# Kernel tuning notes

Measured on AMD Instinct MI355X. Metric: run time of the kernel, lower is better.

Reference implementation:

```python
import jax, jax.numpy as jnp
import numpy as np

N_NODES = 100000
N_EDGES = 1600000
IN_FEATS = 128
OUT_FEATS = 128


def setup_inputs() -> dict:
    key = jax.random.key(0)
    k1, k2, k3, k4, k5 = jax.random.split(key, 5)
    feature = jax.random.normal(k1, (N_NODES, IN_FEATS), dtype=jnp.float32)
    src = jax.random.randint(k2, (N_EDGES,), 0, N_NODES, dtype=jnp.int64)
    dst = jax.random.randint(k3, (N_EDGES,), 0, N_NODES, dtype=jnp.int64)
    # nn.Linear default init: U(-1/sqrt(in), 1/sqrt(in)); randn scaled is fine for a numeric baseline
    bound = 1.0 / np.sqrt(IN_FEATS)
    W = jax.random.uniform(k4, (OUT_FEATS, IN_FEATS), dtype=jnp.float32, minval=-bound, maxval=bound)
    b = jax.random.uniform(k5, (OUT_FEATS,), dtype=jnp.float32, minval=-bound, maxval=bound)
    return {"feature": feature, "src": src, "dst": dst, "W": W, "b": b}


def reference(feature, src, dst, W, b):
    # message passing: copy source feature along each edge, sum into destination node
    agg = jax.ops.segment_sum(feature[src], dst, num_segments=N_NODES)  # [N, in_feats]
    # node apply: ReLU(Linear(h))
    return jax.nn.relu(agg @ W.T + b)  # [N, out_feats]
```

## Files before the change

kernel.cpp:

```cpp
#include <hip/hip_runtime.h>

#define N_NODES 100000
#define N_EDGES 1600000
#define F 128

#define NB    1563
#define NBP2  2048
#define CAP   1280
#define CHUNK 8192

#define BIN_BLOCKS   196
#define HGEMM_BLOCKS 782
#define FRONT_GRID_LIN (BIN_BLOCKS + HGEMM_BLOCKS)

#define LDP  136
#define SMEM_BYTES 77824

typedef __bf16  bf16x8 __attribute__((ext_vector_type(8)));
typedef float   f32x4  __attribute__((ext_vector_type(4)));

__device__ inline unsigned short f32_to_bf16(float f) {
    unsigned u = __builtin_bit_cast(unsigned, f);
    u += 0x7FFFu + ((u >> 16) & 1u);
    return (unsigned short)(u >> 16);
}
__device__ inline unsigned pack_bf16x2(float lo, float hi) {
    return (unsigned)f32_to_bf16(lo) | ((unsigned)f32_to_bf16(hi) << 16);
}
__device__ inline void addrow(float* acc, const uint4 v) {
    acc[0] += __builtin_bit_cast(float, v.x << 16);
    acc[1] += __builtin_bit_cast(float, v.x & 0xFFFF0000u);
    acc[2] += __builtin_bit_cast(float, v.y << 16);
    acc[3] += __builtin_bit_cast(float, v.y & 0xFFFF0000u);
    acc[4] += __builtin_bit_cast(float, v.z << 16);
    acc[5] += __builtin_bit_cast(float, v.z & 0xFFFF0000u);
    acc[6] += __builtin_bit_cast(float, v.w << 16);
    acc[7] += __builtin_bit_cast(float, v.w & 0xFFFF0000u);
}

__global__ __launch_bounds__(1024) void gcn_init(
    const float* __restrict__ W, unsigned short* __restrict__ Wbf,
    int* __restrict__ gcur)
{
    const int i = blockIdx.x * 1024 + threadIdx.x;
    Wbf[i] = f32_to_bf16(W[i]);
    if (i < 1600) gcur[i] = 0;
}

__global__ __launch_bounds__(1024) void gcn_front_lin(
    const float* __restrict__ feat, const unsigned short* __restrict__ Wbf,
    const int* __restrict__ src, const int* __restrict__ dst,
    int* __restrict__ gcur, unsigned* __restrict__ bins,
    unsigned short* __restrict__ H)
{
    __shared__ __align__(16) unsigned char smem[SMEM_BYTES];

    const int tid = threadIdx.x;
    const int bx  = blockIdx.x;

    if (bx >= BIN_BLOCKS) {
        unsigned short* Alds = (unsigned short*)smem;
        unsigned short* Wlds = Alds + 128 * LDP;
        const int row0 = (bx - BIN_BLOCKS) * 128;

        #pragma unroll
        for (int i = 0; i < 2; ++i) {
            const int c = tid + i * 1024;
            const int r = c >> 4, cc = c & 15;
            *(uint4*)&Wlds[r * LDP + cc * 8] = *(const uint4*)&Wbf[c * 8];
        }
        #pragma unroll
        for (int i = 0; i < 4; ++i) {
            const int c = tid + i * 1024;
            const int r = c >> 5, cc = c & 31;
            int gr = row0 + r; if (gr > N_NODES - 1) gr = N_NODES - 1;
            const float4 v = *(const float4*)(feat + (size_t)gr * F + cc * 4);
            uint2 p; p.x = pack_bf16x2(v.x, v.y); p.y = pack_bf16x2(v.z, v.w);
            *(uint2*)&Alds[r * LDP + cc * 4] = p;
        }
        __syncthreads();

        const int lane = tid & 63, wv = tid >> 6;
        const int lr = lane & 15, lq = lane >> 4;
        const int wr = wv & 7;
        const int wc = wv >> 3;

        f32x4 acc[4] = {};
        #pragma unroll
        for (int kk = 0; kk < 4; ++kk) {
            const bf16x8 a = __builtin_bit_cast(bf16x8,
                *(const uint4*)&Alds[(wr * 16 + lr) * LDP + kk * 32 + lq * 8]);
            #pragma unroll
            for (int n2 = 0; n2 < 4; ++n2) {
                const bf16x8 w = __builtin_bit_cast(bf16x8,
                    *(const uint4*)&Wlds[((wc * 4 + n2) * 16 + lr) * LDP + kk * 32 + lq * 8]);
                acc[n2] = __builtin_amdgcn_mfma_f32_16x16x32_bf16(a, w, acc[n2], 0, 0, 0);
            }
        }
        __syncthreads();

        #pragma unroll
        for (int rg = 0; rg < 4; ++rg) {
            const int r = wr * 16 + lq * 4 + rg;
            #pragma unroll
            for (int n2 = 0; n2 < 4; ++n2)
                Alds[r * LDP + (wc * 4 + n2) * 16 + lr] = f32_to_bf16(acc[n2][rg]);
        }
        __syncthreads();

        #pragma unroll
        for (int i = 0; i < 2; ++i) {
            const int c = tid + i * 1024;
            const int r = c >> 4, cc = c & 15;
            const int gr = row0 + r;
            if (gr < N_NODES)
                *(uint4*)(H + (size_t)gr * F + cc * 8) = *(const uint4*)&Alds[r * LDP + cc * 8];
        }
        return;
    }

    unsigned*       cnt    = (unsigned*)smem;
    unsigned*       off    = cnt + NBP2;
    int*            gbase  = (int*)(off + NBP2);
    unsigned*       staged = (unsigned*)(gbase + NBP2);
    unsigned short* sbk    = (unsigned short*)(staged + CHUNK);
    unsigned*       scan   = (unsigned*)(sbk + CHUNK);

    const int e0 = bx * CHUNK;

    #pragma unroll
    for (int i = 0; i < 2; ++i) cnt[tid + i * 1024] = 0;
    __syncthreads();

    int sv[8], dv[8];
    #pragma unroll
    for (int i = 0; i < 8; ++i) {
        const int e = e0 + tid + i * 1024;
        if (e < N_EDGES) {
            sv[i] = src[e];
            dv[i] = dst[e];
            atomicAdd(&cnt[dv[i] >> 6], 1u);
        } else dv[i] = -1;
    }
    __syncthreads();

    const int lane = tid & 63, wid = tid >> 6;
    const unsigned s = cnt[2 * tid] + cnt[2 * tid + 1];
    unsigned v = s;
    #pragma unroll
    for (int o = 1; o < 64; o <<= 1) {
        const unsigned t = __shfl_up(v, o, 64);
        if (lane >= o) v += t;
    }
    if (lane == 63) scan[wid] = v;
    __syncthreads();
    if (tid < 16) {
        const unsigned w = scan[tid];
        unsigned x = w;
        #pragma unroll
        for (int o = 1; o < 16; o <<= 1) {
            const unsigned t = __shfl_up(x, o, 16);
            if (tid >= o) x += t;
        }
        scan[tid] = x - w;
        if (tid == 15) scan[16] = x;
    }
    __syncthreads();
    const unsigned incl = v + scan[wid];
    const unsigned run  = incl - s;
    off[2 * tid]     = run;
    off[2 * tid + 1] = run + cnt[2 * tid];
    __syncthreads();

    #pragma unroll
    for (int i = 0; i < 8; ++i) {
        if (dv[i] >= 0) {
            const int bk = dv[i] >> 6;
            const unsigned w = (unsigned)sv[i] | ((unsigned)(dv[i] & 63) << 17);
            const unsigned p = atomicAdd(&off[bk], 1u);
            staged[p] = w;
            sbk[p] = (unsigned short)bk;
        }
    }
    __syncthreads();

    #pragma unroll
    for (int i = 0; i < 2; ++i) {
        const int bk = 2 * tid + i;
        if (bk < NB && cnt[bk] > 0)
            gbase[bk] = atomicAdd(&gcur[bk], (int)cnt[bk]);
    }
    __syncthreads();

    const int c_tot = (int)scan[16];
    for (int p = tid; p < c_tot; p += 1024) {
        const int bk = sbk[p];
        const int gp = gbase[bk] + (p - (int)(off[bk] - cnt[bk]));
        if (gp < CAP) bins[(size_t)bk * CAP + gp] = staged[p];
    }
}

__global__ __launch_bounds__(512) void gcn_accum_lin(
    const int* __restrict__ gcur,
    const unsigned* __restrict__ bins,
    const unsigned short* __restrict__ H,
    const float* __restrict__ b,
    float* __restrict__ out)
{
    __shared__ unsigned tmp[CAP];
    __shared__ unsigned list[CAP];
    __shared__ int cnt64[64], scn[64], pos64[64], cur64[64];
    __shared__ int nextn;

    const int tid = threadIdx.x;
    const int bkt = blockIdx.x;

    int c = gcur[bkt]; if (c > CAP) c = CAP;
    const unsigned* bb = bins + (size_t)bkt * CAP;

    for (int i = tid; i < c; i += 512) tmp[i] = bb[i];
    if (tid < 64) cnt64[tid] = 0;
    __syncthreads();

    for (int i = tid; i < c; i += 512) atomicAdd(&cnt64[(tmp[i] >> 17) & 63], 1);
    __syncthreads();

    if (tid < 64) scn[tid] = cnt64[tid];
    __syncthreads();
    #pragma unroll
    for (int o = 1; o < 64; o <<= 1) {
        int t = 0;
        if (tid < 64 && tid >= o) t = scn[tid - o];
        __syncthreads();
        if (tid < 64) scn[tid] += t;
        __syncthreads();
    }
    if (tid < 64) {
        const int st = scn[tid] - cnt64[tid];
        pos64[tid] = st;
        cur64[tid] = st;
    }
    if (tid == 0) nextn = 0;
    __syncthreads();

    for (int i = tid; i < c; i += 512) {
        const unsigned w = tmp[i];
        const int p = atomicAdd(&cur64[(w >> 17) & 63], 1);
        list[p] = w;
    }
    __syncthreads();

    const int grp  = tid >> 4;
    const int sl   = tid & 15;
    const int lane = tid & 63;
    const int n0   = bkt * 64;

    for (;;) {
        int myn = 0;
        if (sl == 0) myn = atomicAdd(&nextn, 1);
        myn = __shfl(myn, lane & 48, 64);
        if (myn >= 64) break;

        const int st = pos64[myn];
        const int en = st + cnt64[myn];

        float a0[8] = {0,0,0,0,0,0,0,0};
        float a1[8] = {0,0,0,0,0,0,0,0};
        int k = st;
        for (; k + 7 < en; k += 8) {
            const unsigned w0 = list[k],     w1 = list[k + 1];
            const unsigned w2 = list[k + 2], w3 = list[k + 3];
            const unsigned w4 = list[k + 4], w5 = list[k + 5];
            const unsigned w6 = list[k + 6], w7 = list[k + 7];
            const uint4 v0 = *(const uint4*)(H + (size_t)(w0 & 0x1FFFF) * F + sl * 8);
            const uint4 v1 = *(const uint4*)(H + (size_t)(w1 & 0x1FFFF) * F + sl * 8);
            const uint4 v2 = *(const uint4*)(H + (size_t)(w2 & 0x1FFFF) * F + sl * 8);
            const uint4 v3 = *(const uint4*)(H + (size_t)(w3 & 0x1FFFF) * F + sl * 8);
            const uint4 v4 = *(const uint4*)(H + (size_t)(w4 & 0x1FFFF) * F + sl * 8);
            const uint4 v5 = *(const uint4*)(H + (size_t)(w5 & 0x1FFFF) * F + sl * 8);
            const uint4 v6 = *(const uint4*)(H + (size_t)(w6 & 0x1FFFF) * F + sl * 8);
            const uint4 v7 = *(const uint4*)(H + (size_t)(w7 & 0x1FFFF) * F + sl * 8);
            addrow(a0, v0); addrow(a1, v1); addrow(a0, v2); addrow(a1, v3);
            addrow(a0, v4); addrow(a1, v5); addrow(a0, v6); addrow(a1, v7);
        }
        for (; k + 3 < en; k += 4) {
            const unsigned w0 = list[k],     w1 = list[k + 1];
            const unsigned w2 = list[k + 2], w3 = list[k + 3];
            const uint4 v0 = *(const uint4*)(H + (size_t)(w0 & 0x1FFFF) * F + sl * 8);
            const uint4 v1 = *(const uint4*)(H + (size_t)(w1 & 0x1FFFF) * F + sl * 8);
            const uint4 v2 = *(const uint4*)(H + (size_t)(w2 & 0x1FFFF) * F + sl * 8);
            const uint4 v3 = *(const uint4*)(H + (size_t)(w3 & 0x1FFFF) * F + sl * 8);
            addrow(a0, v0); addrow(a1, v1); addrow(a0, v2); addrow(a1, v3);
        }
        for (; k < en; ++k) {
            const unsigned w0 = list[k];
            const uint4 v0 = *(const uint4*)(H + (size_t)(w0 & 0x1FFFF) * F + sl * 8);
            addrow(a0, v0);
        }
        #pragma unroll
        for (int q = 0; q < 8; ++q) a0[q] += a1[q];

        const int n = n0 + myn;
        if (n < N_NODES) {
            const float4 b0 = *(const float4*)(b + sl * 8);
            const float4 b1 = *(const float4*)(b + sl * 8 + 4);
            float4 o0, o1;
            o0.x = fmaxf(a0[0] + b0.x, 0.0f);
            o0.y = fmaxf(a0[1] + b0.y, 0.0f);
            o0.z = fmaxf(a0[2] + b0.z, 0.0f);
            o0.w = fmaxf(a0[3] + b0.w, 0.0f);
            o1.x = fmaxf(a0[4] + b1.x, 0.0f);
            o1.y = fmaxf(a0[5] + b1.y, 0.0f);
            o1.z = fmaxf(a0[6] + b1.z, 0.0f);
            o1.w = fmaxf(a0[7] + b1.w, 0.0f);
            float* orow = out + (size_t)n * F + sl * 8;
            *(float4*)orow = o0;
            *(float4*)(orow + 4) = o1;
        }
    }
}

#define FEAT_BLOCKS 3125
#define WCONV_BLOCKS 16
#define FRONT_GRID  (BIN_BLOCKS + FEAT_BLOCKS + WCONV_BLOCKS)

__global__ __launch_bounds__(1024) void gcn_front(
    const float* __restrict__ feat, const float* __restrict__ W,
    const int* __restrict__ src, const int* __restrict__ dst,
    int* __restrict__ gcur, unsigned* __restrict__ bins,
    unsigned short* __restrict__ Wbf, float* __restrict__ out)
{
    __shared__ unsigned cnt[NBP2];
    __shared__ unsigned off[NBP2];
    __shared__ int      gbase[NBP2];
    __shared__ unsigned staged[CHUNK];
    __shared__ unsigned short sbk[CHUNK];
    __shared__ unsigned scan[1024];

    const int tid = threadIdx.x;
    const int bx  = blockIdx.x;

    if (bx >= BIN_BLOCKS) {
        const int rb = bx - BIN_BLOCKS;
        if (rb < FEAT_BLOCKS) {
            const int t = rb * 1024 + tid;
            const float4 v = *(const float4*)(feat + (size_t)t * 4);
            uint2 p;
            p.x = pack_bf16x2(v.x, v.y);
            p.y = pack_bf16x2(v.z, v.w);
            const int n = t >> 5, q = t & 31;
            *(uint2*)((char*)out + (size_t)n * 512 + q * 8) = p;
        } else {
            const int i = (rb - FEAT_BLOCKS) * 1024 + tid;
            Wbf[i] = f32_to_bf16(W[i]);
        }
        return;
    }

    const int e0 = bx * CHUNK;

    #pragma unroll
    for (int i = 0; i < 2; ++i) cnt[tid + i * 1024] = 0;
    __syncthreads();

    int sv[8], dv[8];
    #pragma unroll
    for (int i = 0; i < 8; ++i) {
        const int e = e0 + tid + i * 1024;
        if (e < N_EDGES) {
            sv[i] = src[e];
            dv[i] = dst[e];
            atomicAdd(&cnt[dv[i] >> 6], 1u);
        } else dv[i] = -1;
    }
    __syncthreads();

    const unsigned s = cnt[2 * tid] + cnt[2 * tid + 1];
    scan[tid] = s;
    __syncthreads();
    for (int o = 1; o < 1024; o <<= 1) {
        const unsigned t = (tid >= o) ? scan[tid - o] : 0;
        __syncthreads();
        scan[tid] += t;
        __syncthreads();
    }
    const unsigned run = scan[tid] - s;
    off[2 * tid]     = run;
    off[2 * tid + 1] = run + cnt[2 * tid];
    __syncthreads();

    #pragma unroll
    for (int i = 0; i < 8; ++i) {
        if (dv[i] >= 0) {
            const int bk = dv[i] >> 6;
            const unsigned w = (unsigned)sv[i] | ((unsigned)(dv[i] & 63) << 17);
            const unsigned p = atomicAdd(&off[bk], 1u);
            staged[p] = w;
            sbk[p] = (unsigned short)bk;
        }
    }
    __syncthreads();

    #pragma unroll
    for (int i = 0; i < 2; ++i) {
        const int bk = 2 * tid + i;
        if (bk < NB && cnt[bk] > 0)
            gbase[bk] = atomicAdd(&gcur[bk], (int)cnt[bk]);
    }
    __syncthreads();

    const int c_tot = (int)scan[1023];
    for (int p = tid; p < c_tot; p += 1024) {
        const int bk = sbk[p];
        const int gp = gbase[bk] + (p - (int)(off[bk] - cnt[bk]));
        if (gp < CAP) bins[(size_t)bk * CAP + gp] = staged[p];
    }
}

__global__ __launch_bounds__(512) void gcn_accum2(
    const int* __restrict__ gcur,
    const unsigned* __restrict__ bins,
    float* __restrict__ out)
{
    __shared__ unsigned tmp[CAP];
    __shared__ unsigned list[CAP];
    __shared__ int cnt64[64], scn[64], pos64[64], cur64[64];

    const int tid = threadIdx.x;
    const int bkt = blockIdx.x;

    int c = gcur[bkt]; if (c > CAP) c = CAP;
    const unsigned* bb = bins + (size_t)bkt * CAP;

    for (int i = tid; i < c; i += 512) tmp[i] = bb[i];
    if (tid < 64) cnt64[tid] = 0;
    __syncthreads();

    for (int i = tid; i < c; i += 512) atomicAdd(&cnt64[(tmp[i] >> 17) & 63], 1);
    __syncthreads();

    if (tid < 64) scn[tid] = cnt64[tid];
    __syncthreads();
    #pragma unroll
    for (int o = 1; o < 64; o <<= 1) {
        int t = 0;
        if (tid < 64 && tid >= o) t = scn[tid - o];
        __syncthreads();
        if (tid < 64) scn[tid] += t;
        __syncthreads();
    }
    if (tid < 64) {
        const int st = scn[tid] - cnt64[tid];
        pos64[tid] = st;
        cur64[tid] = st;
    }
    __syncthreads();

    for (int i = tid; i < c; i += 512) {
        const unsigned w = tmp[i];
        const int p = atomicAdd(&cur64[(w >> 17) & 63], 1);
        list[p] = w;
    }
    __syncthreads();

    const int grp = tid >> 4;
    const int sl  = tid & 15;
    const int n0  = bkt * 64;

    #pragma unroll
    for (int ni = 0; ni < 2; ++ni) {
        const int l  = grp * 2 + ni;
        const int st = pos64[l];
        const int en = st + cnt64[l];

        float a0[8] = {0,0,0,0,0,0,0,0};
        float a1[8] = {0,0,0,0,0,0,0,0};
        int k = st;
        for (; k + 3 < en; k += 4) {
            const unsigned w0 = list[k],     w1 = list[k + 1];
            const unsigned w2 = list[k + 2], w3 = list[k + 3];
            const uint4 v0 = *(const uint4*)((const char*)out + (size_t)(w0 & 0x1FFFF) * 512 + sl * 16);
            const uint4 v1 = *(const uint4*)((const char*)out + (size_t)(w1 & 0x1FFFF) * 512 + sl * 16);
            const uint4 v2 = *(const uint4*)((const char*)out + (size_t)(w2 & 0x1FFFF) * 512 + sl * 16);
            const uint4 v3 = *(const uint4*)((const char*)out + (size_t)(w3 & 0x1FFFF) * 512 + sl * 16);
            addrow(a0, v0); addrow(a1, v1); addrow(a0, v2); addrow(a1, v3);
        }
        for (; k < en; ++k) {
            const unsigned w0 = list[k];
            const uint4 v0 = *(const uint4*)((const char*)out + (size_t)(w0 & 0x1FFFF) * 512 + sl * 16);
            addrow(a0, v0);
        }
        #pragma unroll
        for (int q = 0; q < 8; ++q) a0[q] += a1[q];

        const int n = n0 + l;
        if (n < N_NODES) {
            uint4 o;
            o.x = pack_bf16x2(a0[0], a0[1]);
            o.y = pack_bf16x2(a0[2], a0[3]);
            o.z = pack_bf16x2(a0[4], a0[5]);
            o.w = pack_bf16x2(a0[6], a0[7]);
            *(uint4*)((char*)out + (size_t)n * 512 + 256 + sl * 16) = o;
        }
    }
}

#define MT   128

__global__ __launch_bounds__(256) void gcn_gemm_mfma(
    float* __restrict__ out,
    const unsigned short* __restrict__ Wbf,
    const float* __restrict__ b)
{
    __shared__ unsigned short Alds[MT * LDP];
    __shared__ unsigned short Wlds[F * LDP];

    const int tid  = threadIdx.x;
    const int row0 = blockIdx.x * MT;

    #pragma unroll
    for (int i = 0; i < 8; ++i) {
        const int c = tid + i * 256;
        const int r = c >> 4, cc = c & 15;
        *(uint4*)&Wlds[r * LDP + cc * 8] = *(const uint4*)&Wbf[c * 8];
    }
    #pragma unroll
    for (int i = 0; i < 8; ++i) {
        const int c = tid + i * 256;
        const int r = c >> 4, cc = c & 15;
        int gr = row0 + r; if (gr > N_NODES - 1) gr = N_NODES - 1;
        const uint4 v = *(const uint4*)((const char*)out + (size_t)gr * 512 + 256 + cc * 16);
        *(uint4*)&Alds[r * LDP + cc * 8] = v;
    }
    __syncthreads();

    const int lane = tid & 63;
    const int wv   = tid >> 6;
    const int lr   = lane & 15;
    const int lq   = lane >> 4;

    f32x4 acc[2][8] = {};
    #pragma unroll
    for (int kk = 0; kk < 4; ++kk) {
        bf16x8 a[2], w[8];
        #pragma unroll
        for (int i = 0; i < 2; ++i)
            a[i] = __builtin_bit_cast(bf16x8,
                *(const uint4*)&Alds[(wv * 32 + i * 16 + lr) * LDP + kk * 32 + lq * 8]);
        #pragma unroll
        for (int n = 0; n < 8; ++n)
            w[n] = __builtin_bit_cast(bf16x8,
                *(const uint4*)&Wlds[(n * 16 + lr) * LDP + kk * 32 + lq * 8]);
        #pragma unroll
        for (int i = 0; i < 2; ++i)
            #pragma unroll
            for (int n = 0; n < 8; ++n)
                acc[i][n] = __builtin_amdgcn_mfma_f32_16x16x32_bf16(a[i], w[n], acc[i][n], 0, 0, 0);
    }

    float bias[8];
    #pragma unroll
    for (int n = 0; n < 8; ++n) bias[n] = b[n * 16 + lr];

    #pragma unroll
    for (int i = 0; i < 2; ++i) {
        const int rbase = wv * 32 + i * 16 + lq * 4;
        #pragma unroll
        for (int rg = 0; rg < 4; ++rg) {
            const int gr = row0 + rbase + rg;
            if (gr < N_NODES) {
                float* orow = out + (size_t)gr * F;
                #pragma unroll
                for (int n = 0; n < 8; ++n) {
                    const float v = acc[i][n][rg] + bias[n];
                    orow[n * 16 + lr] = v > 0.0f ? v : 0.0f;
                }
            }
        }
    }
}

__global__ __launch_bounds__(256) void gcn_scatter(
    const float* __restrict__ feat,
    const int* __restrict__ src, const int* __restrict__ dst,
    float* __restrict__ agg)
{
    const int sub  = threadIdx.x >> 5;
    const int lane = threadIdx.x & 31;
    const long long e = (long long)blockIdx.x * 8 + sub;
    if (e >= N_EDGES) return;
    const int s = src[e], d = dst[e];
    const float4 v = *(const float4*)(feat + (size_t)s * F + lane * 4);
    float* ar = agg + (size_t)d * F + lane * 4;
    unsafeAtomicAdd(ar + 0, v.x);
    unsafeAtomicAdd(ar + 1, v.y);
    unsafeAtomicAdd(ar + 2, v.z);
    unsafeAtomicAdd(ar + 3, v.w);
}

#define GR  64
#define LDW 132
__global__ __launch_bounds__(256) void gcn_gemm_relu(
    float* __restrict__ agg_out,
    const float* __restrict__ W, const float* __restrict__ b)
{
    __shared__ float Wl[F][LDW];
    __shared__ float At[GR][LDW];
    const int tid = threadIdx.x;
    const long long row0 = (long long)blockIdx.x * GR;
    #pragma unroll
    for (int i = 0; i < 64; ++i) {
        const int e = tid + i * 256;
        Wl[e >> 7][e & 127] = W[e];
    }
    #pragma unroll
    for (int i = 0; i < 32; ++i) {
        const int e = tid + i * 256;
        const int r = e >> 7, k2 = e & 127;
        const long long gr = row0 + r;
        At[r][k2] = (gr < N_NODES) ? agg_out[gr * F + k2] : 0.0f;
    }
    __syncthreads();
    const int tx = tid & 15, ty = tid >> 4, r0 = ty * 4;
    float acc[4][8];
    #pragma unroll
    for (int r = 0; r < 4; ++r)
        #pragma unroll
        for (int m = 0; m < 8; ++m) acc[r][m] = 0.0f;
    for (int k0 = 0; k0 < F; k0 += 4) {
        float4 a[4], w[8];
        #pragma unroll
        for (int r = 0; r < 4; ++r) a[r] = *(const float4*)&At[r0 + r][k0];
        #pragma unroll
        for (int m = 0; m < 8; ++m) w[m] = *(const float4*)&Wl[tx + 16 * m][k0];
        #pragma unroll
        for (int r = 0; r < 4; ++r)
            #pragma unroll
            for (int m = 0; m < 8; ++m)
                acc[r][m] += a[r].x * w[m].x + a[r].y * w[m].y
                           + a[r].z * w[m].z + a[r].w * w[m].w;
    }
    float bias[8];
    #pragma unroll
    for (int m = 0; m < 8; ++m) bias[m] = b[tx + 16 * m];
    __syncthreads();
    #pragma unroll
    for (int r = 0; r < 4; ++r) {
        const long long gr = row0 + r0 + r;
        if (gr < N_NODES) {
            float* orow = agg_out + gr * F;
            #pragma unroll
            for (int m = 0; m < 8; ++m) {
                const float v = acc[r][m] + bias[m];
                orow[tx + 16 * m] = v > 0.0f ? v : 0.0f;
            }
        }
    }
}

extern "C" void kernel_launch(void* const* d_in, const int* in_sizes, int n_in,
                              void* d_out, int out_size, void* d_ws, size_t ws_size,
                              hipStream_t stream) {
    const float* feat = (const float*)d_in[0];
    const int*   src  = (const int*)d_in[1];
    const int*   dst  = (const int*)d_in[2];
    const float* W    = (const float*)d_in[3];
    const float* b    = (const float*)d_in[4];
    float* out = (float*)d_out;

    const size_t ws_lin = 1600u * 4 + (size_t)NB * CAP * 4
                        + (size_t)N_NODES * F * 2 + (size_t)F * F * 2;
    const size_t ws_old = 1600u * 4 + (size_t)NB * CAP * 4 + (size_t)F * F * 2;

    if (ws_size >= ws_lin) {
        int* gcur = (int*)d_ws;
        unsigned* bins = (unsigned*)(gcur + 1600);
        unsigned short* H = (unsigned short*)(bins + (size_t)NB * CAP);
        unsigned short* Wbf = H + (size_t)N_NODES * F;

        gcn_init     <<<16, 1024, 0, stream>>>(W, Wbf, gcur);
        gcn_front_lin<<<FRONT_GRID_LIN, 1024, 0, stream>>>(feat, Wbf, src, dst, gcur, bins, H);
        gcn_accum_lin<<<NB, 512, 0, stream>>>(gcur, bins, H, b, out);
    } else if (ws_size >= ws_old) {
        int* gcur = (int*)d_ws;
        unsigned* bins = (unsigned*)(gcur + 1600);
        unsigned short* Wbf = (unsigned short*)(bins + (size_t)NB * CAP);

        hipMemsetAsync(gcur, 0, NB * sizeof(int), stream);
        gcn_front   <<<FRONT_GRID, 1024, 0, stream>>>(feat, W, src, dst, gcur, bins, Wbf, out);
        gcn_accum2  <<<NB, 512, 0, stream>>>(gcur, bins, out);
        gcn_gemm_mfma<<<(N_NODES + MT - 1) / MT, 256, 0, stream>>>(out, Wbf, b);
    } else {
        hipMemsetAsync(out, 0, (size_t)N_NODES * F * sizeof(float), stream);
        gcn_scatter<<<N_EDGES / 8, 256, 0, stream>>>(feat, src, dst, out);
        gcn_gemm_relu<<<(N_NODES + GR - 1) / GR, 256, 0, stream>>>(out, W, b);
    }
}
```

Before: 187.4 us.

## Drop init kernel, convert W in-block, make accum kernel persistent with work stealing

Removes the separate W-to-bf16 init kernel: each H-GEMM block converts W from fp32 itself, and the bucket counters are zeroed with a memset. The accumulate kernel becomes persistent with 1024 blocks that claim buckets through an atomic counter stored in gcur[1599], replacing the shared-memory scan with a wave shuffle scan. Nontemporal loads and stores are added for the streamed data. The intent is to cut launch overhead and tail imbalance, at the cost of redundant W conversion in every GEMM block.

Result: slower. 195.8 us (+4.5%).

```diff
diff --git a/kernel.cpp b/kernel.cpp
--- a/kernel.cpp
+++ b/kernel.cpp
@@ -8,10 +8,12 @@
 #define NBP2  2048
 #define CAP   1280
 #define CHUNK 8192
+#define BCUR  1599
 
 #define BIN_BLOCKS   196
 #define HGEMM_BLOCKS 782
 #define FRONT_GRID_LIN (BIN_BLOCKS + HGEMM_BLOCKS)
+#define ACC_GRID     1024
 
 #define LDP  136
 #define SMEM_BYTES 77824
@@ -38,17 +40,8 @@
     acc[7] += __builtin_bit_cast(float, v.w & 0xFFFF0000u);
 }
 
-__global__ __launch_bounds__(1024) void gcn_init(
-    const float* __restrict__ W, unsigned short* __restrict__ Wbf,
-    int* __restrict__ gcur)
-{
-    const int i = blockIdx.x * 1024 + threadIdx.x;
-    Wbf[i] = f32_to_bf16(W[i]);
-    if (i < 1600) gcur[i] = 0;
-}
-
 __global__ __launch_bounds__(1024) void gcn_front_lin(
-    const float* __restrict__ feat, const unsigned short* __restrict__ Wbf,
+    const float* __restrict__ feat, const float* __restrict__ W,
     const int* __restrict__ src, const int* __restrict__ dst,
     int* __restrict__ gcur, unsigned* __restrict__ bins,
     unsigned short* __restrict__ H)
@@ -64,18 +57,21 @@
         const int row0 = (bx - BIN_BLOCKS) * 128;
 
         #pragma unroll
-        for (int i = 0; i < 2; ++i) {
+        for (int i = 0; i < 4; ++i) {
             const int c = tid + i * 1024;
-            const int r = c >> 4, cc = c & 15;
-            *(uint4*)&Wlds[r * LDP + cc * 8] = *(const uint4*)&Wbf[c * 8];
+            const int r = c >> 5, cc = c & 31;
+            const f32x4 v = *(const f32x4*)(W + (size_t)c * 4);
+            uint2 p; p.x = pack_bf16x2(v[0], v[1]); p.y = pack_bf16x2(v[2], v[3]);
+            *(uint2*)&Wlds[r * LDP + cc * 4] = p;
         }
         #pragma unroll
         for (int i = 0; i < 4; ++i) {
             const int c = tid + i * 1024;
             const int r = c >> 5, cc = c & 31;
             int gr = row0 + r; if (gr > N_NODES - 1) gr = N_NODES - 1;
-            const float4 v = *(const float4*)(feat + (size_t)gr * F + cc * 4);
-            uint2 p; p.x = pack_bf16x2(v.x, v.y); p.y = pack_bf16x2(v.z, v.w);
+            const f32x4 v = __builtin_nontemporal_load(
+                                 (const f32x4*)(feat + (size_t)gr * F + cc * 4));
+            uint2 p; p.x = pack_bf16x2(v[0], v[1]); p.y = pack_bf16x2(v[2], v[3]);
             *(uint2*)&Alds[r * LDP + cc * 4] = p;
         }
         __syncthreads();
@@ -201,7 +197,7 @@
 }
 
 __global__ __launch_bounds__(512) void gcn_accum_lin(
-    const int* __restrict__ gcur,
+    int* __restrict__ gcur,
     const unsigned* __restrict__ bins,
     const unsigned short* __restrict__ H,
     const float* __restrict__ b,
@@ -209,113 +205,120 @@
 {
     __shared__ unsigned tmp[CAP];
     __shared__ unsigned list[CAP];
-    __shared__ int cnt64[64], scn[64], pos64[64], cur64[64];
+    __shared__ int cnt64[64], pos64[64], cur64[64];
+    __shared__ int sbkt;
     __shared__ int nextn;
 
-    const int tid = threadIdx.x;
-    const int bkt = blockIdx.x;
-
-    int c = gcur[bkt]; if (c > CAP) c = CAP;
-    const unsigned* bb = bins + (size_t)bkt * CAP;
-
-    for (int i = tid; i < c; i += 512) tmp[i] = bb[i];
-    if (tid < 64) cnt64[tid] = 0;
-    __syncthreads();
-
-    for (int i = tid; i < c; i += 512) atomicAdd(&cnt64[(tmp[i] >> 17) & 63], 1);
-    __syncthreads();
-
-    if (tid < 64) scn[tid] = cnt64[tid];
-    __syncthreads();
-    #pragma unroll
-    for (int o = 1; o < 64; o <<= 1) {
-        int t = 0;
-        if (tid < 64 && tid >= o) t = scn[tid - o];
-        __syncthreads();
-        if (tid < 64) scn[tid] += t;
-        __syncthreads();
-    }
-    if (tid < 64) {
-        const int st = scn[tid] - cnt64[tid];
-        pos64[tid] = st;
-        cur64[tid] = st;
-    }
-    if (tid == 0) nextn = 0;
-    __syncthreads();
-
-    for (int i = tid; i < c; i += 512) {
-        const unsigned w = tmp[i];
-        const int p = atomicAdd(&cur64[(w >> 17) & 63], 1);
-        list[p] = w;
-    }
-    __syncthreads();
-
-    const int grp  = tid >> 4;
+    const int tid  = threadIdx.x;
+    const int lane = tid & 63;
     const int sl   = tid & 15;
-    const int lane = tid & 63;
-    const int n0   = bkt * 64;
+
+    const f32x4 b0 = *(const f32x4*)(b + sl * 8);
+    const f32x4 b1 = *(const f32x4*)(b + sl * 8 + 4);
 
     for (;;) {
-        int myn = 0;
-        if (sl == 0) myn = atomicAdd(&nextn, 1);
-        myn = __shfl(myn, lane & 48, 64);
-        if (myn >= 64) break;
-
-        const int st = pos64[myn];
-        const int en = st + cnt64[myn];
-
-        float a0[8] = {0,0,0,0,0,0,0,0};
-        float a1[8] = {0,0,0,0,0,0,0,0};
-        int k = st;
-        for (; k + 7 < en; k += 8) {
-            const unsigned w0 = list[k],     w1 = list[k + 1];
-            const unsigned w2 = list[k + 2], w3 = list[k + 3];
-            const unsigned w4 = list[k + 4], w5 = list[k + 5];
-            const unsigned w6 = list[k + 6], w7 = list[k + 7];
-            const uint4 v0 = *(const uint4*)(H + (size_t)(w0 & 0x1FFFF) * F + sl * 8);
-            const uint4 v1 = *(const uint4*)(H + (size_t)(w1 & 0x1FFFF) * F + sl * 8);
-            const uint4 v2 = *(const uint4*)(H + (size_t)(w2 & 0x1FFFF) * F + sl * 8);
-            const uint4 v3 = *(const uint4*)(H + (size_t)(w3 & 0x1FFFF) * F + sl * 8);
-            const uint4 v4 = *(const uint4*)(H + (size_t)(w4 & 0x1FFFF) * F + sl * 8);
-            const uint4 v5 = *(const uint4*)(H + (size_t)(w5 & 0x1FFFF) * F + sl * 8);
-            const uint4 v6 = *(const uint4*)(H + (size_t)(w6 & 0x1FFFF) * F + sl * 8);
-            const uint4 v7 = *(const uint4*)(H + (size_t)(w7 & 0x1FFFF) * F + sl * 8);
-            addrow(a0, v0); addrow(a1, v1); addrow(a0, v2); addrow(a1, v3);
-            addrow(a0, v4); addrow(a1, v5); addrow(a0, v6); addrow(a1, v7);
-        }
-        for (; k + 3 < en; k += 4) {
-            const unsigned w0 = list[k],     w1 = list[k + 1];
-            const unsigned w2 = list[k + 2], w3 = list[k + 3];
-            const uint4 v0 = *(const uint4*)(H + (size_t)(w0 & 0x1FFFF) * F + sl * 8);
-            const uint4 v1 = *(const uint4*)(H + (size_t)(w1 & 0x1FFFF) * F + sl * 8);
-            const uint4 v2 = *(const uint4*)(H + (size_t)(w2 & 0x1FFFF) * F + sl * 8);
-            const uint4 v3 = *(const uint4*)(H + (size_t)(w3 & 0x1FFFF) * F + sl * 8);
-            addrow(a0, v0); addrow(a1, v1); addrow(a0, v2); addrow(a1, v3);
-        }
-        for (; k < en; ++k) {
-            const unsigned w0 = list[k];
-            const uint4 v0 = *(const uint4*)(H + (size_t)(w0 & 0x1FFFF) * F + sl * 8);
-            addrow(a0, v0);
-        }
-        #pragma unroll
-        for (int q = 0; q < 8; ++q) a0[q] += a1[q];
-
-        const int n = n0 + myn;
-        if (n < N_NODES) {
-            const float4 b0 = *(const float4*)(b + sl * 8);
-            const float4 b1 = *(const float4*)(b + sl * 8 + 4);
-            float4 o0, o1;
-            o0.x = fmaxf(a0[0] + b0.x, 0.0f);
-            o0.y = fmaxf(a0[1] + b0.y, 0.0f);
-            o0.z = fmaxf(a0[2] + b0.z, 0.0f);
-            o0.w = fmaxf(a0[3] + b0.w, 0.0f);
-            o1.x = fmaxf(a0[4] + b1.x, 0.0f);
-            o1.y = fmaxf(a0[5] + b1.y, 0.0f);
-            o1.z = fmaxf(a0[6] + b1.z, 0.0f);
-            o1.w = fmaxf(a0[7] + b1.w, 0.0f);
-            float* orow = out + (size_t)n * F + sl * 8;
-            *(float4*)orow = o0;
-            *(float4*)(orow + 4) = o1;
+        __syncthreads();
+        if (tid == 0) {
+            sbkt  = atomicAdd(&gcur[BCUR], 1);
+            nextn = 0;
+        }
+        __syncthreads();
+        const int bkt = sbkt;
+        if (bkt >= NB) return;
+
+        int c = gcur[bkt]; if (c > CAP) c = CAP;
+        const unsigned* bb = bins + (size_t)bkt * CAP;
+
+        for (int i = tid; i < c; i += 512)
+            tmp[i] = __builtin_nontemporal_load(bb + i);
+        if (tid < 64) cnt64[tid] = 0;
+        __syncthreads();
+
+        for (int i = tid; i < c; i += 512) atomicAdd(&cnt64[(tmp[i] >> 17) & 63], 1);
+        __syncthreads();
+
+        if (tid < 64) {
+            const int cv = cnt64[tid];
+            int x = cv;
+            #pragma unroll
+            for (int o = 1; o < 64; o <<= 1) {
+                const int t = __shfl_up(x, o, 64);
+                if (tid >= o) x += t;
+            }
+            pos64[tid] = x - cv;
+            cur64[tid] = x - cv;
+        }
+        __syncthreads();
+
+        for (int i = tid; i < c; i += 512) {
+            const unsigned w = tmp[i];
+            const int p = atomicAdd(&cur64[(w >> 17) & 63], 1);
+            list[p] = w;
+        }
+        __syncthreads();
+
+        const int n0 = bkt * 64;
+
+        for (;;) {
+            int myn = 0;
+            if (sl == 0) myn = atomicAdd(&nextn, 1);
+            myn = __shfl(myn, lane & 48, 64);
+            if (myn >= 64) break;
+
+            const int st = pos64[myn];
+            const int en = st + cnt64[myn];
+
+            float a0[8] = {0,0,0,0,0,0,0,0};
+            float a1[8] = {0,0,0,0,0,0,0,0};
+            int k = st;
+            for (; k + 7 < en; k += 8) {
+                const unsigned w0 = list[k],     w1 = list[k + 1];
+                const unsigned w2 = list[k + 2], w3 = list[k + 3];
+                const unsigned w4 = list[k + 4], w5 = list[k + 5];
+                const unsigned w6 = list[k + 6], w7 = list[k + 7];
+                const uint4 v0 = *(const uint4*)(H + (size_t)(w0 & 0x1FFFF) * F + sl * 8);
+                const uint4 v1 = *(const uint4*)(H + (size_t)(w1 & 0x1FFFF) * F + sl * 8);
+                const uint4 v2 = *(const uint4*)(H + (size_t)(w2 & 0x1FFFF) * F + sl * 8);
+                const uint4 v3 = *(const uint4*)(H + (size_t)(w3 & 0x1FFFF) * F + sl * 8);
+                const uint4 v4 = *(const uint4*)(H + (size_t)(w4 & 0x1FFFF) * F + sl * 8);
+                const uint4 v5 = *(const uint4*)(H + (size_t)(w5 & 0x1FFFF) * F + sl * 8);
+                const uint4 v6 = *(const uint4*)(H + (size_t)(w6 & 0x1FFFF) * F + sl * 8);
+                const uint4 v7 = *(const uint4*)(H + (size_t)(w7 & 0x1FFFF) * F + sl * 8);
+                addrow(a0, v0); addrow(a1, v1); addrow(a0, v2); addrow(a1, v3);
+                addrow(a0, v4); addrow(a1, v5); addrow(a0, v6); addrow(a1, v7);
+            }
+            for (; k + 3 < en; k += 4) {
+                const unsigned w0 = list[k],     w1 = list[k + 1];
+                const unsigned w2 = list[k + 2], w3 = list[k + 3];
+                const uint4 v0 = *(const uint4*)(H + (size_t)(w0 & 0x1FFFF) * F + sl * 8);
+                const uint4 v1 = *(const uint4*)(H + (size_t)(w1 & 0x1FFFF) * F + sl * 8);
+                const uint4 v2 = *(const uint4*)(H + (size_t)(w2 & 0x1FFFF) * F + sl * 8);
+                const uint4 v3 = *(const uint4*)(H + (size_t)(w3 & 0x1FFFF) * F + sl * 8);
+                addrow(a0, v0); addrow(a1, v1); addrow(a0, v2); addrow(a1, v3);
+            }
+            for (; k < en; ++k) {
+                const unsigned w0 = list[k];
+                const uint4 v0 = *(const uint4*)(H + (size_t)(w0 & 0x1FFFF) * F + sl * 8);
+                addrow(a0, v0);
+            }
+            #pragma unroll
+            for (int q = 0; q < 8; ++q) a0[q] += a1[q];
+
+            const int n = n0 + myn;
+            if (n < N_NODES) {
+                f32x4 o0, o1;
+                o0[0] = fmaxf(a0[0] + b0[0], 0.0f);
+                o0[1] = fmaxf(a0[1] + b0[1], 0.0f);
+                o0[2] = fmaxf(a0[2] + b0[2], 0.0f);
+                o0[3] = fmaxf(a0[3] + b0[3], 0.0f);
+                o1[0] = fmaxf(a0[4] + b1[0], 0.0f);
+                o1[1] = fmaxf(a0[5] + b1[1], 0.0f);
+                o1[2] = fmaxf(a0[6] + b1[2], 0.0f);
+                o1[3] = fmaxf(a0[7] + b1[3], 0.0f);
+                float* orow = out + (size_t)n * F + sl * 8;
+                __builtin_nontemporal_store(o0, (f32x4*)orow);
+                __builtin_nontemporal_store(o1, (f32x4*)(orow + 4));
+            }
         }
     }
 }
@@ -668,19 +671,17 @@
     const float* b    = (const float*)d_in[4];
     float* out = (float*)d_out;
 
-    const size_t ws_lin = 1600u * 4 + (size_t)NB * CAP * 4
-                        + (size_t)N_NODES * F * 2 + (size_t)F * F * 2;
+    const size_t ws_lin = 1600u * 4 + (size_t)NB * CAP * 4 + (size_t)N_NODES * F * 2;
     const size_t ws_old = 1600u * 4 + (size_t)NB * CAP * 4 + (size_t)F * F * 2;
 
     if (ws_size >= ws_lin) {
         int* gcur = (int*)d_ws;
         unsigned* bins = (unsigned*)(gcur + 1600);
         unsigned short* H = (unsigned short*)(bins + (size_t)NB * CAP);
-        unsigned short* Wbf = H + (size_t)N_NODES * F;
-
-        gcn_init     <<<16, 1024, 0, stream>>>(W, Wbf, gcur);
-        gcn_front_lin<<<FRONT_GRID_LIN, 1024, 0, stream>>>(feat, Wbf, src, dst, gcur, bins, H);
-        gcn_accum_lin<<<NB, 512, 0, stream>>>(gcur, bins, H, b, out);
+
+        hipMemsetAsync(gcur, 0, 1600 * sizeof(int), stream);
+        gcn_front_lin<<<FRONT_GRID_LIN, 1024, 0, stream>>>(feat, W, src, dst, gcur, bins, H);
+        gcn_accum_lin<<<ACC_GRID, 512, 0, stream>>>(gcur, bins, H, b, out);
     } else if (ws_size >= ws_old) {
         int* gcur = (int*)d_ws;
         unsigned* bins = (unsigned*)(gcur + 1600);
```
